# Kernel tuning notes

Measured on AMD Instinct MI355X. Metric: run time of the kernel, lower is better.

## Reference

```python
import jax, jax.numpy as jnp
import numpy as np

def setup_inputs() -> dict:
    key = jax.random.key(0)
    k1, k2, k3, k4, k5 = jax.random.split(key, 5)
    H = 1024
    B, T = 32, 1024
    hidden = jax.random.normal(k1, (1, B, H), dtype=jnp.float32)
    encoder_outputs = jax.random.normal(k2, (B, T, H), dtype=jnp.float32)
    # nn.Linear(2H, H): weight [H, 2H], bias [H]
    bound = 1.0 / np.sqrt(2 * H)
    W = jax.random.uniform(k3, (H, 2 * H), minval=-bound, maxval=bound, dtype=jnp.float32)
    b = jax.random.uniform(k4, (H,), minval=-bound, maxval=bound, dtype=jnp.float32)
    v = jax.random.uniform(k5, (H,), dtype=jnp.float32)  # torch.rand
    return {"hidden": hidden, "encoder_outputs": encoder_outputs, "W": W, "b": b, "v": v}

def reference(hidden, encoder_outputs, W, b, v):
    B = hidden.shape[1]
    H = hidden.shape[2]
    h = jnp.transpose(hidden, (1, 0, 2)).reshape(B, -1)  # [B, H]
    # Split Linear(2H->H): cat([h_rep, enc]) @ W.T == h @ Wh.T + enc @ We.T
    Wh, We = W[:, :H], W[:, H:]
    # [B,1,H] + [B,T,H] -> [B,T,H]
    pre = jnp.tanh((h @ Wh.T + b)[:, None, :] + jnp.einsum('bth,gh->btg', encoder_outputs, We))
    energies = jnp.einsum('bth,h->bt', pre, v)  # [B, T]
    return jax.nn.softmax(energies, axis=1)[:, None, :]  # [B, 1, T]
```

## Files before the change

### kernel.cpp

```cpp
#include <hip/hip_runtime.h>
#include <hip/hip_fp16.h>

typedef _Float16 half8   __attribute__((ext_vector_type(8)));
typedef _Float16 half4_t __attribute__((ext_vector_type(4)));
typedef float    f32x4   __attribute__((ext_vector_type(4)));

#define HDIM  1024
#define BATCH 32
#define TLEN  1024
#define M_TOT (BATCH * TLEN)

#define BM 128
#define BN 128
#define BKF 64
#define LDA 40

__global__ void prep_k(const float* __restrict__ W, const float* __restrict__ hidden,
                       const float* __restrict__ bias, _Float16* __restrict__ We16,
                       float* __restrict__ q, float* __restrict__ energ) {
    const int bid = blockIdx.x;
    const int t = threadIdx.x;
    if (bid < 1024) {
        int idx = bid * 256 + t;
        int g  = idx >> 8;
        int k4 = idx & 255;
        float4 f = *reinterpret_cast<const float4*>(W + (size_t)g * 2048 + 1024 + k4 * 4);
        half4_t h;
        h[0] = (_Float16)f.x; h[1] = (_Float16)f.y; h[2] = (_Float16)f.z; h[3] = (_Float16)f.w;
        *reinterpret_cast<half4_t*>(We16 + (size_t)idx * 4) = h;
    } else if (bid < 2048) {
        int g = bid - 1024;
        int wave = t >> 6, lane = t & 63;
        float acc[BATCH];
#pragma unroll
        for (int b = 0; b < BATCH; b++) acc[b] = 0.f;
        const float* wr = W + (size_t)g * 2048;
        for (int h = t; h < HDIM; h += 256) {
            float w = wr[h];
#pragma unroll
            for (int b = 0; b < BATCH; b++) acc[b] = fmaf(w, hidden[b * HDIM + h], acc[b]);
        }
        __shared__ float sm[4 * BATCH];
#pragma unroll
        for (int b = 0; b < BATCH; b++) {
            float s = acc[b];
#pragma unroll
            for (int off = 32; off >= 1; off >>= 1) s += __shfl_xor(s, off);
            if (lane == 0) sm[wave * BATCH + b] = s;
        }
        __syncthreads();
        if (t < BATCH) {
            float s = sm[t] + sm[BATCH + t] + sm[2 * BATCH + t] + sm[3 * BATCH + t];
            q[t * HDIM + g] = s + bias[g];
        }
    } else {
        energ[(bid - 2048) * 256 + t] = 0.f;
    }
}

__global__ void enc_convert_k(const float* __restrict__ enc, _Float16* __restrict__ enc16) {
    size_t i = ((size_t)blockIdx.x * blockDim.x + threadIdx.x) * 8;
    float4 f0 = *reinterpret_cast<const float4*>(enc + i);
    float4 f1 = *reinterpret_cast<const float4*>(enc + i + 4);
    half8 h;
    h[0] = (_Float16)f0.x; h[1] = (_Float16)f0.y; h[2] = (_Float16)f0.z; h[3] = (_Float16)f0.w;
    h[4] = (_Float16)f1.x; h[5] = (_Float16)f1.y; h[6] = (_Float16)f1.z; h[7] = (_Float16)f1.w;
    *reinterpret_cast<half8*>(enc16 + i) = h;
}

__device__ __forceinline__ void async16(const void* g, void* l) {
    __builtin_amdgcn_global_load_lds(
        (const __attribute__((address_space(1))) void*)g,
        (__attribute__((address_space(3))) void*)l, 16, 0, 0);
}

__global__ __launch_bounds__(256)
void attn_gemm_lds_k(const _Float16* __restrict__ enc16,
                     const _Float16* __restrict__ We16,
                     const float* __restrict__ q, const float* __restrict__ v,
                     float* __restrict__ energies) {
    __shared__ _Float16 As[BM * BKF];
    __shared__ _Float16 Bs[BN * BKF];

    const int tid  = threadIdx.x;
    const int id   = blockIdx.x;
    const int xcd  = id & 7;
    const int w    = id >> 3;
    const int m0   = (xcd * 32 + (w >> 3)) * BM;
    const int n0   = (w & 7) * BN;
    const int wave = tid >> 6;
    const int lane = tid & 63;
    const int quad = lane >> 4;
    const int l16  = lane & 15;
    const int wm   = (wave & 1) * 64;
    const int wn   = (wave >> 1) * 64;

    f32x4 acc[4][4];
#pragma unroll
    for (int i = 0; i < 4; i++)
#pragma unroll
        for (int j = 0; j < 4; j++) acc[i][j] = {0.f, 0.f, 0.f, 0.f};

    const int srow = wave * 32 + (lane >> 3);
    const int scol = ((lane & 7) ^ (lane >> 3)) * 8;
    const _Float16* gA = enc16 + (size_t)(m0 + srow) * HDIM + scol;
    const _Float16* gB = We16  + (size_t)(n0 + srow) * HDIM + scol;
    _Float16* lA = As + wave * 2048;
    _Float16* lB = Bs + wave * 2048;
    const size_t istep = (size_t)8 * HDIM;

#pragma unroll
    for (int ii = 0; ii < 4; ii++) {
        async16(gA + ii * istep, lA + ii * 512);
        async16(gB + ii * istep, lB + ii * 512);
    }
    __syncthreads();

    int aoff[2][4], boff[2][4];
#pragma unroll
    for (int s = 0; s < 2; s++)
#pragma unroll
        for (int i = 0; i < 4; i++) {
            int ra = wm + i * 16 + l16;
            int rb = wn + i * 16 + l16;
            aoff[s][i] = ra * BKF + (((s * 4 + quad) ^ (l16 & 7)) * 8);
            boff[s][i] = rb * BKF + (((s * 4 + quad) ^ (l16 & 7)) * 8);
        }

    for (int k0 = 0; k0 < HDIM; k0 += BKF) {
        half8 af[2][4], bf[2][4];
#pragma unroll
        for (int s = 0; s < 2; s++)
#pragma unroll
            for (int i = 0; i < 4; i++) {
                af[s][i] = *reinterpret_cast<const half8*>(&As[aoff[s][i]]);
                bf[s][i] = *reinterpret_cast<const half8*>(&Bs[boff[s][i]]);
            }
        __syncthreads();

        if (k0 + BKF < HDIM) {
            const int kn = k0 + BKF;
#pragma unroll
            for (int ii = 0; ii < 4; ii++) {
                async16(gA + kn + ii * istep, lA + ii * 512);
                async16(gB + kn + ii * istep, lB + ii * 512);
            }
        }

#pragma unroll
        for (int s = 0; s < 2; s++)
#pragma unroll
            for (int mi = 0; mi < 4; mi++)
#pragma unroll
                for (int ni = 0; ni < 4; ni++)
                    acc[mi][ni] = __builtin_amdgcn_mfma_f32_16x16x32_f16(af[s][mi], bf[s][ni], acc[mi][ni], 0, 0, 0);

        __syncthreads();
    }

    const int bidx = m0 >> 10;
    float qv[4], vv[4];
#pragma unroll
    for (int ni = 0; ni < 4; ni++) {
        int g = n0 + wn + ni * 16 + l16;
        qv[ni] = q[bidx * HDIM + g];
        vv[ni] = v[g];
    }
#pragma unroll
    for (int mi = 0; mi < 4; mi++) {
#pragma unroll
        for (int r = 0; r < 4; r++) {
            int row = wm + mi * 16 + quad * 4 + r;
            float s = 0.f;
#pragma unroll
            for (int ni = 0; ni < 4; ni++) {
                float pre = acc[mi][ni][r] + qv[ni];
                float e = __expf(2.f * pre);
                float th = 1.f - 2.f / (e + 1.f);
                s = fmaf(th, vv[ni], s);
            }
            s += __shfl_xor(s, 1);
            s += __shfl_xor(s, 2);
            s += __shfl_xor(s, 4);
            s += __shfl_xor(s, 8);
            if (l16 == 0) atomicAdd(&energies[m0 + row], s);
        }
    }
}

__global__ __launch_bounds__(256, 2)
void attn_gemm_k(const float* __restrict__ enc, const _Float16* __restrict__ We16,
                 const float* __restrict__ q, const float* __restrict__ v,
                 float* __restrict__ energies) {
    __shared__ _Float16 As[BM * LDA];
    __shared__ _Float16 Bs[BN * LDA];

    const int tid  = threadIdx.x;
    const int m0   = blockIdx.x * BM;
    const int n0   = blockIdx.y * BN;
    const int wave = tid >> 6;
    const int lane = tid & 63;
    const int quad = lane >> 4;
    const int l16  = lane & 15;
    const int wm   = (wave & 1) * 64;
    const int wn   = (wave >> 1) * 64;

    const int srow = tid >> 1;
    const int scol = (tid & 1) * 16;

    f32x4 acc[4][4];
#pragma unroll
    for (int i = 0; i < 4; i++)
#pragma unroll
        for (int j = 0; j < 4; j++) acc[i][j] = {0.f, 0.f, 0.f, 0.f};

    const float*    ag = enc  + (size_t)(m0 + srow) * HDIM + scol;
    const _Float16* bg = We16 + (size_t)(n0 + srow) * HDIM + scol;
    _Float16* aw = &As[srow * LDA + scol];
    _Float16* bw = &Bs[srow * LDA + scol];

    for (int k0 = 0; k0 < HDIM; k0 += 32) {
        float4 a0 = *reinterpret_cast<const float4*>(ag + k0 + 0);
        float4 a1 = *reinterpret_cast<const float4*>(ag + k0 + 4);
        float4 a2 = *reinterpret_cast<const float4*>(ag + k0 + 8);
        float4 a3 = *reinterpret_cast<const float4*>(ag + k0 + 12);
        float4 b0 = *reinterpret_cast<const float4*>(bg + k0);
        float4 b1 = *reinterpret_cast<const float4*>(bg + k0 + 8);

        __syncthreads();

        half8 ha0, ha1;
        ha0[0] = (_Float16)a0.x; ha0[1] = (_Float16)a0.y; ha0[2] = (_Float16)a0.z; ha0[3] = (_Float16)a0.w;
        ha0[4] = (_Float16)a1.x; ha0[5] = (_Float16)a1.y; ha0[6] = (_Float16)a1.z; ha0[7] = (_Float16)a1.w;
        ha1[0] = (_Float16)a2.x; ha1[1] = (_Float16)a2.y; ha1[2] = (_Float16)a2.z; ha1[3] = (_Float16)a2.w;
        ha1[4] = (_Float16)a3.x; ha1[5] = (_Float16)a3.y; ha1[6] = (_Float16)a3.z; ha1[7] = (_Float16)a3.w;
        *reinterpret_cast<half8*>(aw)     = ha0;
        *reinterpret_cast<half8*>(aw + 8) = ha1;
        *reinterpret_cast<float4*>(bw)     = b0;
        *reinterpret_cast<float4*>(bw + 8) = b1;

        __syncthreads();

        half8 af[4], bf[4];
#pragma unroll
        for (int i = 0; i < 4; i++) {
            af[i] = *reinterpret_cast<const half8*>(&As[(wm + i * 16 + l16) * LDA + quad * 8]);
            bf[i] = *reinterpret_cast<const half8*>(&Bs[(wn + i * 16 + l16) * LDA + quad * 8]);
        }
#pragma unroll
        for (int mi = 0; mi < 4; mi++)
#pragma unroll
            for (int ni = 0; ni < 4; ni++)
                acc[mi][ni] = __builtin_amdgcn_mfma_f32_16x16x32_f16(af[mi], bf[ni], acc[mi][ni], 0, 0, 0);
    }

    const int bidx = m0 >> 10;
    float qv[4], vv[4];
#pragma unroll
    for (int ni = 0; ni < 4; ni++) {
        int g = n0 + wn + ni * 16 + l16;
        qv[ni] = q[bidx * HDIM + g];
        vv[ni] = v[g];
    }
#pragma unroll
    for (int mi = 0; mi < 4; mi++) {
#pragma unroll
        for (int r = 0; r < 4; r++) {
            int row = wm + mi * 16 + quad * 4 + r;
            float s = 0.f;
#pragma unroll
            for (int ni = 0; ni < 4; ni++) {
                float pre = acc[mi][ni][r] + qv[ni];
                float e = __expf(2.f * pre);
                float th = 1.f - 2.f / (e + 1.f);
                s = fmaf(th, vv[ni], s);
            }
            s += __shfl_xor(s, 1);
            s += __shfl_xor(s, 2);
            s += __shfl_xor(s, 4);
            s += __shfl_xor(s, 8);
            if (l16 == 0) atomicAdd(&energies[m0 + row], s);
        }
    }
}

__global__ void softmax_k(const float* __restrict__ energies, float* __restrict__ out) {
    int b = blockIdx.x;
    int t = threadIdx.x;
    int wave = t >> 6, lane = t & 63;
    __shared__ float smax[4], ssum[4];
    float e[4];
#pragma unroll
    for (int i = 0; i < 4; i++) e[i] = energies[b * TLEN + t + i * 256];
    float m = fmaxf(fmaxf(e[0], e[1]), fmaxf(e[2], e[3]));
#pragma unroll
    for (int off = 32; off >= 1; off >>= 1) m = fmaxf(m, __shfl_xor(m, off));
    if (lane == 0) smax[wave] = m;
    __syncthreads();
    float M = fmaxf(fmaxf(smax[0], smax[1]), fmaxf(smax[2], smax[3]));
    float x[4]; float s = 0.f;
#pragma unroll
    for (int i = 0; i < 4; i++) { x[i] = __expf(e[i] - M); s += x[i]; }
#pragma unroll
    for (int off = 32; off >= 1; off >>= 1) s += __shfl_xor(s, off);
    if (lane == 0) ssum[wave] = s;
    __syncthreads();
    float S = ssum[0] + ssum[1] + ssum[2] + ssum[3];
    float inv = 1.f / S;
#pragma unroll
    for (int i = 0; i < 4; i++) out[b * TLEN + t + i * 256] = x[i] * inv;
}

extern "C" void kernel_launch(void* const* d_in, const int* in_sizes, int n_in,
                              void* d_out, int out_size, void* d_ws, size_t ws_size,
                              hipStream_t stream) {
    const float* hidden = (const float*)d_in[0];
    const float* enc    = (const float*)d_in[1];
    const float* W      = (const float*)d_in[2];
    const float* bias   = (const float*)d_in[3];
    const float* v      = (const float*)d_in[4];
    float* out = (float*)d_out;

    char* ws = (char*)d_ws;
    float*    q     = (float*)ws;
    float*    energ = (float*)(ws + 131072);
    _Float16* We16  = (_Float16*)(ws + 262144);
    _Float16* enc16 = (_Float16*)(ws + 262144 + 2097152);
    const size_t need_fast = 262144 + 2097152 + (size_t)M_TOT * HDIM * 2;

    prep_k<<<dim3(2176), 256, 0, stream>>>(W, hidden, bias, We16, q, energ);
    if (ws_size >= need_fast) {
        enc_convert_k<<<dim3((size_t)M_TOT * HDIM / 8 / 256), 256, 0, stream>>>(enc, enc16);
        attn_gemm_lds_k<<<dim3(2048), 256, 0, stream>>>(enc16, We16, q, v, energ);
    } else {
        attn_gemm_k<<<dim3(256, 8), 256, 0, stream>>>(enc, We16, q, v, energ);
    }
    softmax_k<<<dim3(BATCH), 256, 0, stream>>>(energ, out);
}
```

Baseline: 309.5 us.

## Replace energy atomics with partial-sum buffer and fuse enc conversion into prep

```diff
diff --git a/kernel.cpp b/kernel.cpp
--- a/kernel.cpp
+++ b/kernel.cpp
@@ -16,8 +16,9 @@
 #define LDA 40
 
 __global__ void prep_k(const float* __restrict__ W, const float* __restrict__ hidden,
-                       const float* __restrict__ bias, _Float16* __restrict__ We16,
-                       float* __restrict__ q, float* __restrict__ energ) {
+                       const float* __restrict__ bias, const float* __restrict__ enc,
+                       _Float16* __restrict__ We16, float* __restrict__ q,
+                       _Float16* __restrict__ enc16) {
     const int bid = blockIdx.x;
     const int t = threadIdx.x;
     if (bid < 1024) {
@@ -54,18 +55,14 @@
             q[t * HDIM + g] = s + bias[g];
         }
     } else {
-        energ[(bid - 2048) * 256 + t] = 0.f;
-    }
-}
-
-__global__ void enc_convert_k(const float* __restrict__ enc, _Float16* __restrict__ enc16) {
-    size_t i = ((size_t)blockIdx.x * blockDim.x + threadIdx.x) * 8;
-    float4 f0 = *reinterpret_cast<const float4*>(enc + i);
-    float4 f1 = *reinterpret_cast<const float4*>(enc + i + 4);
-    half8 h;
-    h[0] = (_Float16)f0.x; h[1] = (_Float16)f0.y; h[2] = (_Float16)f0.z; h[3] = (_Float16)f0.w;
-    h[4] = (_Float16)f1.x; h[5] = (_Float16)f1.y; h[6] = (_Float16)f1.z; h[7] = (_Float16)f1.w;
-    *reinterpret_cast<half8*>(enc16 + i) = h;
+        size_t i = ((size_t)(bid - 2048) * 256 + t) * 8;
+        float4 f0 = *reinterpret_cast<const float4*>(enc + i);
+        float4 f1 = *reinterpret_cast<const float4*>(enc + i + 4);
+        half8 h;
+        h[0] = (_Float16)f0.x; h[1] = (_Float16)f0.y; h[2] = (_Float16)f0.z; h[3] = (_Float16)f0.w;
+        h[4] = (_Float16)f1.x; h[5] = (_Float16)f1.y; h[6] = (_Float16)f1.z; h[7] = (_Float16)f1.w;
+        *reinterpret_cast<half8*>(enc16 + i) = h;
+    }
 }
 
 __device__ __forceinline__ void async16(const void* g, void* l) {
@@ -78,7 +75,7 @@
 void attn_gemm_lds_k(const _Float16* __restrict__ enc16,
                      const _Float16* __restrict__ We16,
                      const float* __restrict__ q, const float* __restrict__ v,
-                     float* __restrict__ energies) {
+                     float* __restrict__ energ) {
     __shared__ _Float16 As[BM * BKF];
     __shared__ _Float16 Bs[BN * BKF];
 
@@ -88,6 +85,7 @@
     const int w    = id >> 3;
     const int m0   = (xcd * 32 + (w >> 3)) * BM;
     const int n0   = (w & 7) * BN;
+    const int nblk = w & 7;
     const int wave = tid >> 6;
     const int lane = tid & 63;
     const int quad = lane >> 4;
@@ -159,6 +157,7 @@
     }
 
     const int bidx = m0 >> 10;
+    const int half = wn >> 6;
     float qv[4], vv[4];
 #pragma unroll
     for (int ni = 0; ni < 4; ni++) {
@@ -183,7 +182,7 @@
             s += __shfl_xor(s, 2);
             s += __shfl_xor(s, 4);
             s += __shfl_xor(s, 8);
-            if (l16 == 0) atomicAdd(&energies[m0 + row], s);
+            if (l16 == 0) energ[(size_t)(m0 + row) * 16 + nblk * 2 + half] = s;
         }
     }
 }
@@ -191,7 +190,7 @@
 __global__ __launch_bounds__(256, 2)
 void attn_gemm_k(const float* __restrict__ enc, const _Float16* __restrict__ We16,
                  const float* __restrict__ q, const float* __restrict__ v,
-                 float* __restrict__ energies) {
+                 float* __restrict__ energ) {
     __shared__ _Float16 As[BM * LDA];
     __shared__ _Float16 Bs[BN * LDA];
 
@@ -255,6 +254,7 @@
     }
 
     const int bidx = m0 >> 10;
+    const int half = wn >> 6;
     float qv[4], vv[4];
 #pragma unroll
     for (int ni = 0; ni < 4; ni++) {
@@ -279,19 +279,28 @@
             s += __shfl_xor(s, 2);
             s += __shfl_xor(s, 4);
             s += __shfl_xor(s, 8);
-            if (l16 == 0) atomicAdd(&energies[m0 + row], s);
-        }
-    }
-}
-
-__global__ void softmax_k(const float* __restrict__ energies, float* __restrict__ out) {
+            if (l16 == 0) energ[(size_t)(m0 + row) * 16 + blockIdx.y * 2 + half] = s;
+        }
+    }
+}
+
+__global__ void softmax_k(const float* __restrict__ energ, float* __restrict__ out) {
     int b = blockIdx.x;
     int t = threadIdx.x;
     int wave = t >> 6, lane = t & 63;
     __shared__ float smax[4], ssum[4];
     float e[4];
 #pragma unroll
-    for (int i = 0; i < 4; i++) e[i] = energies[b * TLEN + t + i * 256];
+    for (int i = 0; i < 4; i++) {
+        size_t m = (size_t)b * TLEN + t + i * 256;
+        const float* p = energ + m * 16;
+        f32x4 p0 = *reinterpret_cast<const f32x4*>(p);
+        f32x4 p1 = *reinterpret_cast<const f32x4*>(p + 4);
+        f32x4 p2 = *reinterpret_cast<const f32x4*>(p + 8);
+        f32x4 p3 = *reinterpret_cast<const f32x4*>(p + 12);
+        e[i] = ((p0[0] + p0[1]) + (p0[2] + p0[3])) + ((p1[0] + p1[1]) + (p1[2] + p1[3]))
+             + ((p2[0] + p2[1]) + (p2[2] + p2[3])) + ((p3[0] + p3[1]) + (p3[2] + p3[3]));
+    }
     float m = fmaxf(fmaxf(e[0], e[1]), fmaxf(e[2], e[3]));
 #pragma unroll
     for (int off = 32; off >= 1; off >>= 1) m = fmaxf(m, __shfl_xor(m, off));
@@ -324,15 +333,15 @@
     char* ws = (char*)d_ws;
     float*    q     = (float*)ws;
     float*    energ = (float*)(ws + 131072);
-    _Float16* We16  = (_Float16*)(ws + 262144);
-    _Float16* enc16 = (_Float16*)(ws + 262144 + 2097152);
-    const size_t need_fast = 262144 + 2097152 + (size_t)M_TOT * HDIM * 2;
-
-    prep_k<<<dim3(2176), 256, 0, stream>>>(W, hidden, bias, We16, q, energ);
+    _Float16* We16  = (_Float16*)(ws + 131072 + 2097152);
+    _Float16* enc16 = (_Float16*)(ws + 131072 + 2097152 + 2097152);
+    const size_t need_fast = 131072 + 2097152 + 2097152 + (size_t)M_TOT * HDIM * 2;
+
     if (ws_size >= need_fast) {
-        enc_convert_k<<<dim3((size_t)M_TOT * HDIM / 8 / 256), 256, 0, stream>>>(enc, enc16);
+        prep_k<<<dim3(18432), 256, 0, stream>>>(W, hidden, bias, enc, We16, q, enc16);
         attn_gemm_lds_k<<<dim3(2048), 256, 0, stream>>>(enc16, We16, q, v, energ);
     } else {
+        prep_k<<<dim3(2048), 256, 0, stream>>>(W, hidden, bias, enc, We16, q, enc16);
         attn_gemm_k<<<dim3(256, 8), 256, 0, stream>>>(enc, We16, q, v, energ);
     }
     softmax_k<<<dim3(BATCH), 256, 0, stream>>>(energ, out);
```

After: 297.4 us. 1.04x faster.
